# Kernel optimization log

Hardware: AMD Instinct MI355X
Metric: run time of the kernel (lower is better)

## Reference

```python
import jax, jax.numpy as jnp
from jax import lax
import numpy as np

WIN = 9  # default window [9, 9] in the original module


def _box_sum(x, win):
    """Sum over a win x win window, stride 1, pad win//2 (same as conv2d with ones kernel).
    Implemented separably (two 1D convs) - mathematically identical to the 2D ones-kernel conv.
    x: [B, 1, H, W] float32.
    """
    pad = win // 2
    kh = jnp.ones((1, 1, win, 1), x.dtype)
    kw = jnp.ones((1, 1, 1, win), x.dtype)
    dn = lax.conv_dimension_numbers(x.shape, kh.shape, ('NCHW', 'OIHW', 'NCHW'))
    y = lax.conv_general_dilated(x, kh, (1, 1), [(pad, pad), (0, 0)], dimension_numbers=dn)
    return lax.conv_general_dilated(y, kw, (1, 1), [(0, 0), (pad, pad)], dimension_numbers=dn)


def setup_inputs() -> dict:
    key = jax.random.key(0)
    k1, k2 = jax.random.split(key)
    shape = (32, 1, 512, 512)
    predict = jax.random.uniform(k1, shape, dtype=jnp.float32)
    target = jax.random.uniform(k2, shape, dtype=jnp.float32)
    return {"predict": predict, "target": target}


def reference(predict, target):
    win = WIN
    win_size = jnp.asarray(win * win, jnp.float32)

    I, J = predict, target
    I_sum = _box_sum(I, win)
    J_sum = _box_sum(J, win)
    I2_sum = _box_sum(I * I, win)
    J2_sum = _box_sum(J * J, win)
    IJ_sum = _box_sum(I * J, win)

    u_I = I_sum / win_size
    u_J = J_sum / win_size

    cross = IJ_sum - u_J * I_sum - u_I * J_sum + u_I * u_J * win_size
    I_var = I2_sum - 2.0 * u_I * I_sum + u_I * u_I * win_size
    J_var = J2_sum - 2.0 * u_J * J_sum + u_J * u_J * win_size

    cc = cross * cross / (I_var * J_var + 1e-6)
    return -jnp.mean(cc) + 1.0
```

## Files before the change

kernel.cpp:

```cpp
#include <hip/hip_runtime.h>


#define W 512
#define H 512
#define BH 16
#define NBANDS (H / BH)
#define NT 64

__device__ __forceinline__ float4 ld4(const float* p) {
    return *reinterpret_cast<const float4*>(p);
}

#define DECLBUF(P) float4 P##A0, P##A1, P##B0, P##B1; float P##m

#define LOADR(P, DR) do {                                                    \
    int _r  = y0 + (DR);                                                     \
    int _rc = _r < 0 ? 0 : (_r > (H - 1) ? (H - 1) : _r);                    \
    const float* _ip = Ip + _rc * W + x0;                                    \
    const float* _jp = Jp + _rc * W + x0;                                    \
    P##A0 = ld4(_ip);  P##A1 = ld4(_ip + 4);                                 \
    P##B0 = ld4(_jp);  P##B1 = ld4(_jp + 4);                                 \
    P##m  = (_r == _rc) ? 1.f : 0.f;                                         \
} while (0)

#define PBODY(P, OP)                                                         \
    do {                                                                     \
        float _m = P##m;                                                     \
        float _a0=P##A0.x*_m, _a1=P##A0.y*_m, _a2=P##A0.z*_m, _a3=P##A0.w*_m;\
        float _a4=P##A1.x*_m, _a5=P##A1.y*_m, _a6=P##A1.z*_m, _a7=P##A1.w*_m;\
        float _b0=P##B0.x*_m, _b1=P##B0.y*_m, _b2=P##B0.z*_m, _b3=P##B0.w*_m;\
        float _b4=P##B1.x*_m, _b5=P##B1.y*_m, _b6=P##B1.z*_m, _b7=P##B1.w*_m;\
        v0[0] OP _a0; v0[1] OP _a1; v0[2] OP _a2; v0[3] OP _a3;              \
        v0[4] OP _a4; v0[5] OP _a5; v0[6] OP _a6; v0[7] OP _a7;              \
        v1[0] OP _b0; v1[1] OP _b1; v1[2] OP _b2; v1[3] OP _b3;              \
        v1[4] OP _b4; v1[5] OP _b5; v1[6] OP _b6; v1[7] OP _b7;              \
        v2[0] OP _a0*P##A0.x; v2[1] OP _a1*P##A0.y; v2[2] OP _a2*P##A0.z; v2[3] OP _a3*P##A0.w; \
        v2[4] OP _a4*P##A1.x; v2[5] OP _a5*P##A1.y; v2[6] OP _a6*P##A1.z; v2[7] OP _a7*P##A1.w; \
        v3[0] OP _b0*P##B0.x; v3[1] OP _b1*P##B0.y; v3[2] OP _b2*P##B0.z; v3[3] OP _b3*P##B0.w; \
        v3[4] OP _b4*P##B1.x; v3[5] OP _b5*P##B1.y; v3[6] OP _b6*P##B1.z; v3[7] OP _b7*P##B1.w; \
        v4[0] OP _a0*P##B0.x; v4[1] OP _a1*P##B0.y; v4[2] OP _a2*P##B0.z; v4[3] OP _a3*P##B0.w; \
        v4[4] OP _a4*P##B1.x; v4[5] OP _a5*P##B1.y; v4[6] OP _a6*P##B1.z; v4[7] OP _a7*P##B1.w; \
    } while (0)

#define PADD(P) PBODY(P, +=)
#define PSUB(P) PBODY(P, -=)

#define HLO(vv, h, l7out) do {                                               \
    float _l4 = __shfl_up(vv[4], 1), _l5 = __shfl_up(vv[5], 1);              \
    float _l6 = __shfl_up(vv[6], 1), _l7 = __shfl_up(vv[7], 1);              \
    if (lane == 0) { _l4 = 0.f; _l5 = 0.f; _l6 = 0.f; _l7 = 0.f; }           \
    float _t = (((_l4+_l5)+(_l6+_l7)) + ((vv[0]+vv[1])+(vv[2]+vv[3]))) + vv[4]; \
    h[0] = _t;                                                               \
    _t += vv[5] - _l4; h[1] = _t;                                            \
    _t += vv[6] - _l5; h[2] = _t;                                            \
    _t += vv[7] - _l6; h[3] = _t;                                            \
    l7out = _l7;                                                             \
} while (0)

#define HHI(vv, h3in, l7in, h) do {                                          \
    float _r0 = __shfl_down(vv[0], 1), _r1 = __shfl_down(vv[1], 1);          \
    float _r2 = __shfl_down(vv[2], 1), _r3 = __shfl_down(vv[3], 1);          \
    if (lane == 63) { _r0 = 0.f; _r1 = 0.f; _r2 = 0.f; _r3 = 0.f; }          \
    float _t = (h3in) + _r0 - (l7in); h[0] = _t;                             \
    _t += _r1 - vv[0]; h[1] = _t;                                            \
    _t += _r2 - vv[1]; h[2] = _t;                                            \
    _t += _r3 - vv[2]; h[3] = _t;                                            \
} while (0)

#define CC4(h0a, h1a, h2a, h3a, h4a) do {                                    \
    _Pragma("unroll")                                                        \
    for (int _c = 0; _c < 4; ++_c) {                                         \
        float _Is = h0a[_c], _Js = h1a[_c];                                  \
        float _u  = _Is * inv81;                                             \
        float _cr = h4a[_c] - _u * _Js;                                      \
        float _Iv = h2a[_c] - _u * _Is;                                      \
        float _Jv = h3a[_c] - (_Js * inv81) * _Js;                           \
        cc_acc += (_cr * _cr) * __builtin_amdgcn_rcpf(_Iv * _Jv + 1e-6f);    \
    }                                                                        \
} while (0)

#define EPI() do {                                                           \
    float h0[4], h1[4], h2[4], h3[4], h4[4];                                 \
    float s0, s1, s2, s3, s4;                                                \
    HLO(v0, h0, s0); HLO(v1, h1, s1); HLO(v2, h2, s2);                       \
    HLO(v3, h3, s3); HLO(v4, h4, s4);                                        \
    CC4(h0, h1, h2, h3, h4);                                                 \
    float e0 = h0[3], e1 = h1[3], e2 = h2[3], e3 = h3[3], e4 = h4[3];        \
    HHI(v0, e0, s0, h0); HHI(v1, e1, s1, h1); HHI(v2, e2, s2, h2);           \
    HHI(v3, e3, s3, h3); HHI(v4, e4, s4, h4);                                \
    CC4(h0, h1, h2, h3, h4);                                                 \
} while (0)

#define STEPL(AB, SB, DR) do { PADD(AB); EPI(); PSUB(SB); LOADR(SB, DR); } while (0)
#define STEPN(AB, SB)     do { PADD(AB); EPI(); PSUB(SB); } while (0)

__global__ __launch_bounds__(NT)
void ncc_main(const float* __restrict__ I, const float* __restrict__ J,
              float* __restrict__ partials) {
    const int lane = threadIdx.x & 63;

    const int nblk = gridDim.x;
    const int g = (blockIdx.x & 7) * (nblk >> 3) + (blockIdx.x >> 3);

    const int b    = g >> 5;
    const int band = g & (NBANDS - 1);
    const int y0   = band * BH;
    const float* Ip = I + (size_t)b * (H * W);
    const float* Jp = J + (size_t)b * (H * W);
    const int x0 = lane * 8;

    float v0[8], v1[8], v2[8], v3[8], v4[8];
    #pragma unroll
    for (int k = 0; k < 8; ++k) { v0[k]=0.f; v1[k]=0.f; v2[k]=0.f; v3[k]=0.f; v4[k]=0.f; }

    float cc_acc = 0.f;
    const float inv81 = 1.f / 81.f;

    DECLBUF(B0); DECLBUF(B1); DECLBUF(B2); DECLBUF(B3); DECLBUF(B4);
    DECLBUF(B5); DECLBUF(B6); DECLBUF(B7); DECLBUF(B8); DECLBUF(B9);

    LOADR(B0, -4); LOADR(B1, -3); LOADR(B2, -2); LOADR(B3, -1);
    LOADR(B4,  0); LOADR(B5,  1); LOADR(B6,  2); LOADR(B7,  3);
    LOADR(B8,  4); LOADR(B9,  5);

    PADD(B0); PADD(B1); PADD(B2); PADD(B3);
    PADD(B4); PADD(B5); PADD(B6); PADD(B7);

    STEPL(B8, B0,  6);
    STEPL(B9, B1,  7);
    STEPL(B0, B2,  8);
    STEPL(B1, B3,  9);
    STEPL(B2, B4, 10);
    STEPL(B3, B5, 11);
    STEPL(B4, B6, 12);
    STEPL(B5, B7, 13);
    STEPL(B6, B8, 14);
    STEPL(B7, B9, 15);
    STEPL(B8, B0, 16);
    STEPL(B9, B1, 17);
    STEPL(B0, B2, 18);
    STEPL(B1, B3, 19);
    STEPN(B2, B4);
    STEPN(B3, B5);

    #pragma unroll
    for (int off = 32; off > 0; off >>= 1)
        cc_acc += __shfl_down(cc_acc, off, 64);
    if (lane == 0) partials[blockIdx.x] = cc_acc;
}

__global__ __launch_bounds__(256)
void ncc_finish(const float* __restrict__ partials, float* __restrict__ out,
                int n, float inv_total) {
    float v = 0.f;
    for (int i = threadIdx.x; i < n; i += blockDim.x) v += partials[i];
    #pragma unroll
    for (int off = 32; off > 0; off >>= 1)
        v += __shfl_down(v, off, 64);
    __shared__ float wsum[4];
    if ((threadIdx.x & 63) == 0) wsum[threadIdx.x >> 6] = v;
    __syncthreads();
    if (threadIdx.x == 0) {
        float t = (wsum[0] + wsum[1]) + (wsum[2] + wsum[3]);
        out[0] = 1.0f - t * inv_total;
    }
}

extern "C" void kernel_launch(void* const* d_in, const int* in_sizes, int n_in,
                              void* d_out, int out_size, void* d_ws, size_t ws_size,
                              hipStream_t stream) {
    const float* I = (const float*)d_in[0];
    const float* J = (const float*)d_in[1];
    float* out = (float*)d_out;
    float* partials = (float*)d_ws;

    const int n = in_sizes[0];
    const int B = n / (H * W);
    const int nblocks = B * NBANDS;

    ncc_main<<<nblocks, NT, 0, stream>>>(I, J, partials);
    ncc_finish<<<1, 256, 0, stream>>>(partials, out, nblocks, 1.0f / (float)n);
}
```

Measured before the change: 105.8 us.

## Keep sliding-window rows in an LDS ring instead of ten register buffers

```diff
diff --git a/kernel.cpp b/kernel.cpp
--- a/kernel.cpp
+++ b/kernel.cpp
@@ -11,11 +11,11 @@
     return *reinterpret_cast<const float4*>(p);
 }
 
-#define DECLBUF(P) float4 P##A0, P##A1, P##B0, P##B1; float P##m
-
-#define LOADR(P, DR) do {                                                    \
-    int _r  = y0 + (DR);                                                     \
-    int _rc = _r < 0 ? 0 : (_r > (H - 1) ? (H - 1) : _r);                    \
+#define DECLP(P) float4 P##A0, P##A1, P##B0, P##B1; float P##m
+
+#define LOADP(P, ROW) do {                                                   \
+    int _r  = (ROW);                                                         \
+    int _rc = _r < 0 ? 0 : (_r > H - 1 ? H - 1 : _r);                        \
     const float* _ip = Ip + _rc * W + x0;                                    \
     const float* _jp = Jp + _rc * W + x0;                                    \
     P##A0 = ld4(_ip);  P##A1 = ld4(_ip + 4);                                 \
@@ -23,27 +23,47 @@
     P##m  = (_r == _rc) ? 1.f : 0.f;                                         \
 } while (0)
 
-#define PBODY(P, OP)                                                         \
-    do {                                                                     \
-        float _m = P##m;                                                     \
-        float _a0=P##A0.x*_m, _a1=P##A0.y*_m, _a2=P##A0.z*_m, _a3=P##A0.w*_m;\
-        float _a4=P##A1.x*_m, _a5=P##A1.y*_m, _a6=P##A1.z*_m, _a7=P##A1.w*_m;\
-        float _b0=P##B0.x*_m, _b1=P##B0.y*_m, _b2=P##B0.z*_m, _b3=P##B0.w*_m;\
-        float _b4=P##B1.x*_m, _b5=P##B1.y*_m, _b6=P##B1.z*_m, _b7=P##B1.w*_m;\
-        v0[0] OP _a0; v0[1] OP _a1; v0[2] OP _a2; v0[3] OP _a3;              \
-        v0[4] OP _a4; v0[5] OP _a5; v0[6] OP _a6; v0[7] OP _a7;              \
-        v1[0] OP _b0; v1[1] OP _b1; v1[2] OP _b2; v1[3] OP _b3;              \
-        v1[4] OP _b4; v1[5] OP _b5; v1[6] OP _b6; v1[7] OP _b7;              \
-        v2[0] OP _a0*P##A0.x; v2[1] OP _a1*P##A0.y; v2[2] OP _a2*P##A0.z; v2[3] OP _a3*P##A0.w; \
-        v2[4] OP _a4*P##A1.x; v2[5] OP _a5*P##A1.y; v2[6] OP _a6*P##A1.z; v2[7] OP _a7*P##A1.w; \
-        v3[0] OP _b0*P##B0.x; v3[1] OP _b1*P##B0.y; v3[2] OP _b2*P##B0.z; v3[3] OP _b3*P##B0.w; \
-        v3[4] OP _b4*P##B1.x; v3[5] OP _b5*P##B1.y; v3[6] OP _b6*P##B1.z; v3[7] OP _b7*P##B1.w; \
-        v4[0] OP _a0*P##B0.x; v4[1] OP _a1*P##B0.y; v4[2] OP _a2*P##B0.z; v4[3] OP _a3*P##B0.w; \
-        v4[4] OP _a4*P##B1.x; v4[5] OP _a5*P##B1.y; v4[6] OP _a6*P##B1.z; v4[7] OP _a7*P##B1.w; \
-    } while (0)
-
-#define PADD(P) PBODY(P, +=)
-#define PSUB(P) PBODY(P, -=)
+#define MADDW(P, BASE) do {                                                  \
+    float _m = P##m;                                                         \
+    float _f0=P##A0.x*_m, _f1=P##A0.y*_m, _f2=P##A0.z*_m, _f3=P##A0.w*_m;    \
+    float _f4=P##A1.x*_m, _f5=P##A1.y*_m, _f6=P##A1.z*_m, _f7=P##A1.w*_m;    \
+    float _g0=P##B0.x*_m, _g1=P##B0.y*_m, _g2=P##B0.z*_m, _g3=P##B0.w*_m;    \
+    float _g4=P##B1.x*_m, _g5=P##B1.y*_m, _g6=P##B1.z*_m, _g7=P##B1.w*_m;    \
+    v0[0]+=_f0; v0[1]+=_f1; v0[2]+=_f2; v0[3]+=_f3;                          \
+    v0[4]+=_f4; v0[5]+=_f5; v0[6]+=_f6; v0[7]+=_f7;                          \
+    v1[0]+=_g0; v1[1]+=_g1; v1[2]+=_g2; v1[3]+=_g3;                          \
+    v1[4]+=_g4; v1[5]+=_g5; v1[6]+=_g6; v1[7]+=_g7;                          \
+    v2[0]+=_f0*_f0; v2[1]+=_f1*_f1; v2[2]+=_f2*_f2; v2[3]+=_f3*_f3;          \
+    v2[4]+=_f4*_f4; v2[5]+=_f5*_f5; v2[6]+=_f6*_f6; v2[7]+=_f7*_f7;          \
+    v3[0]+=_g0*_g0; v3[1]+=_g1*_g1; v3[2]+=_g2*_g2; v3[3]+=_g3*_g3;          \
+    v3[4]+=_g4*_g4; v3[5]+=_g5*_g5; v3[6]+=_g6*_g6; v3[7]+=_g7*_g7;          \
+    v4[0]+=_f0*_g0; v4[1]+=_f1*_g1; v4[2]+=_f2*_g2; v4[3]+=_f3*_g3;          \
+    v4[4]+=_f4*_g4; v4[5]+=_f5*_g5; v4[6]+=_f6*_g6; v4[7]+=_f7*_g7;          \
+    *(float4*)((BASE)      ) = make_float4(_f0,_f1,_f2,_f3);                 \
+    *(float4*)((BASE) + 256) = make_float4(_f4,_f5,_f6,_f7);                 \
+    *(float4*)((BASE) + 512) = make_float4(_g0,_g1,_g2,_g3);                 \
+    *(float4*)((BASE) + 768) = make_float4(_g4,_g5,_g6,_g7);                 \
+} while (0)
+
+#define RSUB_READ(BASE) do {                                                 \
+    rs0 = *(const float4*)((BASE)      );                                    \
+    rs1 = *(const float4*)((BASE) + 256);                                    \
+    rs2 = *(const float4*)((BASE) + 512);                                    \
+    rs3 = *(const float4*)((BASE) + 768);                                    \
+} while (0)
+
+#define VSUBR() do {                                                         \
+    v0[0]-=rs0.x; v0[1]-=rs0.y; v0[2]-=rs0.z; v0[3]-=rs0.w;                  \
+    v0[4]-=rs1.x; v0[5]-=rs1.y; v0[6]-=rs1.z; v0[7]-=rs1.w;                  \
+    v1[0]-=rs2.x; v1[1]-=rs2.y; v1[2]-=rs2.z; v1[3]-=rs2.w;                  \
+    v1[4]-=rs3.x; v1[5]-=rs3.y; v1[6]-=rs3.z; v1[7]-=rs3.w;                  \
+    v2[0]-=rs0.x*rs0.x; v2[1]-=rs0.y*rs0.y; v2[2]-=rs0.z*rs0.z; v2[3]-=rs0.w*rs0.w; \
+    v2[4]-=rs1.x*rs1.x; v2[5]-=rs1.y*rs1.y; v2[6]-=rs1.z*rs1.z; v2[7]-=rs1.w*rs1.w; \
+    v3[0]-=rs2.x*rs2.x; v3[1]-=rs2.y*rs2.y; v3[2]-=rs2.z*rs2.z; v3[3]-=rs2.w*rs2.w; \
+    v3[4]-=rs3.x*rs3.x; v3[5]-=rs3.y*rs3.y; v3[6]-=rs3.z*rs3.z; v3[7]-=rs3.w*rs3.w; \
+    v4[0]-=rs0.x*rs2.x; v4[1]-=rs0.y*rs2.y; v4[2]-=rs0.z*rs2.z; v4[3]-=rs0.w*rs2.w; \
+    v4[4]-=rs1.x*rs3.x; v4[5]-=rs1.y*rs3.y; v4[6]-=rs1.z*rs3.z; v4[7]-=rs1.w*rs3.w; \
+} while (0)
 
 #define HLO(vv, h, l7out) do {                                               \
     float _l4 = __shfl_up(vv[4], 1), _l5 = __shfl_up(vv[5], 1);              \
@@ -91,13 +111,12 @@
     CC4(h0, h1, h2, h3, h4);                                                 \
 } while (0)
 
-#define STEPL(AB, SB, DR) do { PADD(AB); EPI(); PSUB(SB); LOADR(SB, DR); } while (0)
-#define STEPN(AB, SB)     do { PADD(AB); EPI(); PSUB(SB); } while (0)
-
 __global__ __launch_bounds__(NT)
 void ncc_main(const float* __restrict__ I, const float* __restrict__ J,
               float* __restrict__ partials) {
-    const int lane = threadIdx.x & 63;
+    __shared__ float ring[8][4][NT][4];
+
+    const int lane = threadIdx.x;
 
     const int nblk = gridDim.x;
     const int g = (blockIdx.x & 7) * (nblk >> 3) + (blockIdx.x >> 3);
@@ -116,32 +135,37 @@
     float cc_acc = 0.f;
     const float inv81 = 1.f / 81.f;
 
-    DECLBUF(B0); DECLBUF(B1); DECLBUF(B2); DECLBUF(B3); DECLBUF(B4);
-    DECLBUF(B5); DECLBUF(B6); DECLBUF(B7); DECLBUF(B8); DECLBUF(B9);
-
-    LOADR(B0, -4); LOADR(B1, -3); LOADR(B2, -2); LOADR(B3, -1);
-    LOADR(B4,  0); LOADR(B5,  1); LOADR(B6,  2); LOADR(B7,  3);
-    LOADR(B8,  4); LOADR(B9,  5);
-
-    PADD(B0); PADD(B1); PADD(B2); PADD(B3);
-    PADD(B4); PADD(B5); PADD(B6); PADD(B7);
-
-    STEPL(B8, B0,  6);
-    STEPL(B9, B1,  7);
-    STEPL(B0, B2,  8);
-    STEPL(B1, B3,  9);
-    STEPL(B2, B4, 10);
-    STEPL(B3, B5, 11);
-    STEPL(B4, B6, 12);
-    STEPL(B5, B7, 13);
-    STEPL(B6, B8, 14);
-    STEPL(B7, B9, 15);
-    STEPL(B8, B0, 16);
-    STEPL(B9, B1, 17);
-    STEPL(B0, B2, 18);
-    STEPL(B1, B3, 19);
-    STEPN(B2, B4);
-    STEPN(B3, B5);
+    float* const myring = &ring[0][0][lane][0];
+
+    DECLP(P); DECLP(Q);
+
+    LOADP(P, y0 - 4); LOADP(Q, y0 - 3);
+    MADDW(P, myring + 0 * 1024); LOADP(P, y0 - 2);
+    MADDW(Q, myring + 1 * 1024); LOADP(Q, y0 - 1);
+    MADDW(P, myring + 2 * 1024); LOADP(P, y0 + 0);
+    MADDW(Q, myring + 3 * 1024); LOADP(Q, y0 + 1);
+    MADDW(P, myring + 4 * 1024); LOADP(P, y0 + 2);
+    MADDW(Q, myring + 5 * 1024); LOADP(Q, y0 + 3);
+    MADDW(P, myring + 6 * 1024);
+    MADDW(Q, myring + 7 * 1024);
+
+    LOADP(P, y0 + 4); LOADP(Q, y0 + 5);
+
+    float4 rs0, rs1, rs2, rs3;
+    #pragma unroll 2
+    for (int i = 0; i < 16; ++i) {
+        float* sb = myring + (i & 7) * 1024;
+        RSUB_READ(sb);
+        if ((i & 1) == 0) {
+            MADDW(P, sb);
+            if (i < 14) LOADP(P, y0 + 6 + i);
+        } else {
+            MADDW(Q, sb);
+            if (i < 14) LOADP(Q, y0 + 6 + i);
+        }
+        EPI();
+        VSUBR();
+    }
 
     #pragma unroll
     for (int off = 32; off > 0; off >>= 1)
```

Measured after the change: 108.2 us. +2.3%, slower.
